# Kernel tuning notes

Measured on AMD Instinct MI355X. Metric: run time of the kernel, lower is better.

## Reference

```python
import jax, jax.numpy as jnp
import numpy as np
from jax import lax

B, C_IN, IMG, P, HID = 128, 3, 224, 16, 768
HW = (IMG // P) ** 2  # 196 patches


def setup_inputs() -> dict:
    key = jax.random.key(0)
    k1, k2, k3, k4 = jax.random.split(key, 4)
    x = jax.random.normal(k1, (B, C_IN, IMG, IMG), dtype=jnp.float32)
    # conv weight init scale ~ kaiming-ish, value irrelevant for correctness
    W = jax.random.normal(k2, (HID, C_IN, P, P), dtype=jnp.float32) * 0.02
    b = jax.random.normal(k3, (HID,), dtype=jnp.float32) * 0.02
    # per-sample random permutation of patch positions (the pixel shuffle)
    perm = jax.vmap(lambda k: jax.random.permutation(k, HW))(jax.random.split(k4, B)).astype(jnp.int32)
    return {"x": x, "W": W, "b": b, "perm": perm}


def reference(x, W, b, perm):
    # patchify conv: kernel_size == stride == P, no padding
    enc = lax.conv_general_dilated(
        x, W, window_strides=(P, P), padding="VALID",
        dimension_numbers=("NCHW", "OIHW", "NCHW"),
    ) + b[None, :, None, None]                      # [B, HID, H', W']
    Bc, Cc, Hc, Wc = enc.shape
    enc = enc.reshape(Bc, Cc, Hc * Wc).transpose(0, 2, 1)   # [B, HW, HID]
    # per-sample patch shuffle: shuffled[i, j] = enc[i, perm[i, j]]
    shuffled = jnp.take_along_axis(enc, perm[:, :, None], axis=1)
    return shuffled
```

## Files before the change

### kernel.cpp

```cpp
#include <hip/hip_runtime.h>
#include <hip/hip_bf16.h>

#define BATCH  128
#define HWN    196
#define HIDN   768
#define KN     768
#define IMGSZ  224
#define IMG2   (224*224)
#define MTOT   (BATCH*HWN)

#define BM 128
#define BN 128
#define BK 32

typedef __attribute__((ext_vector_type(8))) short bf16x8;
typedef __attribute__((ext_vector_type(4))) float floatx4;

#define GP(p) ((const __attribute__((address_space(1))) void*)(p))
#define SP(p) ((__attribute__((address_space(3))) void*)(p))

static __device__ __forceinline__ short f2bf(float f) {
    __hip_bfloat16 h = __float2bfloat16(f);
    return __builtin_bit_cast(short, h);
}

static __device__ __forceinline__ bf16x8 cvt8(const float* __restrict__ src) {
    float4 f0 = *(const float4*)(src);
    float4 f1 = *(const float4*)(src + 4);
    bf16x8 v;
    v[0]=f2bf(f0.x); v[1]=f2bf(f0.y); v[2]=f2bf(f0.z); v[3]=f2bf(f0.w);
    v[4]=f2bf(f1.x); v[5]=f2bf(f1.y); v[6]=f2bf(f1.z); v[7]=f2bf(f1.w);
    return v;
}

__global__ __launch_bounds__(256)
void prep_A(const float* __restrict__ x, const int* __restrict__ perm,
            unsigned short* __restrict__ A)
{
    const int idx = blockIdx.x * 256 + threadIdx.x;
    const int gr  = idx / 48;
    const int seg = idx - gr * 48;
    const int b   = gr / HWN;
    const int p   = perm[gr];
    const int py  = p / 14, px = p - py * 14;
    const int c   = seg >> 4;
    const int iy  = seg & 15;

    const float* src = x + (size_t)b * 3 * IMG2 + (size_t)c * IMG2
                         + (size_t)(py * 16 + iy) * IMGSZ + px * 16;
    bf16x8 v0 = cvt8(src);
    bf16x8 v1 = cvt8(src + 8);
    unsigned short* dst = A + (size_t)gr * KN + seg * 16;
    *(bf16x8*)(dst)     = v0;
    *(bf16x8*)(dst + 8) = v1;
}

__global__ __launch_bounds__(256)
void prep_W(const float* __restrict__ W, unsigned short* __restrict__ Wb)
{
    const int idx = blockIdx.x * 256 + threadIdx.x;
    const float* src = W + (size_t)idx * 8;
    *(bf16x8*)(Wb + (size_t)idx * 8) = cvt8(src);
}

__global__ __launch_bounds__(256, 5)
void gemm(const unsigned short* __restrict__ A, const unsigned short* __restrict__ Wb,
          const float* __restrict__ bias, float* __restrict__ out)
{
    __shared__ __align__(16) unsigned short As[2][BM * BK];
    __shared__ __align__(16) unsigned short Bs[2][BN * BK];

    const int tid = threadIdx.x;

    const int L   = blockIdx.x;
    const int xcd = L & 7;
    const int s   = L >> 3;
    int grp, t;
    if (xcd < 4)        { grp = xcd;     t = s; }
    else if (s < 144)   { grp = xcd;     t = s; }
    else                { grp = xcd - 4; t = 147 + (s - 144); }
    const int bm0 = (grp < 4) ? grp * 25 : 100 + (grp - 4) * 24;
    const int bm  = bm0 + t / 6;
    const int bn  = t % 6;

    const int srow = tid >> 2;
    const int sseg = tid & 3;
    const unsigned short* ga = A  + (size_t)(bm * BM + srow) * KN + sseg * 8;
    const unsigned short* gb = Wb + (size_t)(bn * BN + srow) * KN + sseg * 8;

    const int lane = tid & 63;
    const int wave = tid >> 6;
    const int wm = (wave >> 1) * 64;
    const int wn = (wave & 1) * 64;
    const int lr = lane & 15;
    const int lq = lane >> 4;

    floatx4 acc[4][4] = {};

    auto issue = [&](int k0, int b) {
        __builtin_amdgcn_global_load_lds(GP(ga + k0),           SP(&As[b][tid * 8]),        16, 0, 0);
        __builtin_amdgcn_global_load_lds(GP(ga + 64 * KN + k0), SP(&As[b][2048 + tid * 8]), 16, 0, 0);
        __builtin_amdgcn_global_load_lds(GP(gb + k0),           SP(&Bs[b][tid * 8]),        16, 0, 0);
        __builtin_amdgcn_global_load_lds(GP(gb + 64 * KN + k0), SP(&Bs[b][2048 + tid * 8]), 16, 0, 0);
    };
    auto compute = [&](int b) {
        bf16x8 bfrag[4];
        #pragma unroll
        for (int j = 0; j < 4; ++j)
            bfrag[j] = *(const bf16x8*)&Bs[b][(wn + j * 16 + lr) * BK + lq * 8];
        #pragma unroll
        for (int i = 0; i < 4; ++i) {
            bf16x8 afrag = *(const bf16x8*)&As[b][(wm + i * 16 + lr) * BK + lq * 8];
            #pragma unroll
            for (int j = 0; j < 4; ++j)
                acc[i][j] = __builtin_amdgcn_mfma_f32_16x16x32_bf16(
                                bfrag[j], afrag, acc[i][j], 0, 0, 0);
        }
    };

    issue(0, 0);
    for (int k0 = 0; k0 < KN; k0 += 2 * BK) {
        __syncthreads();
        if (k0 + BK < KN) issue(k0 + BK, 1);
        compute(0);
        __syncthreads();
        if (k0 + 2 * BK < KN) issue(k0 + 2 * BK, 0);
        compute(1);
    }

    #pragma unroll
    for (int j = 0; j < 4; ++j) {
        const int gc0 = bn * BN + wn + j * 16 + lq * 4;
        const float4 bv = *(const float4*)&bias[gc0];
        #pragma unroll
        for (int i = 0; i < 4; ++i) {
            const int grow = bm * BM + wm + i * 16 + lr;
            float4 v;
            v.x = acc[i][j][0] + bv.x;
            v.y = acc[i][j][1] + bv.y;
            v.z = acc[i][j][2] + bv.z;
            v.w = acc[i][j][3] + bv.w;
            *(float4*)(out + (size_t)grow * HIDN + gc0) = v;
        }
    }
}

extern "C" void kernel_launch(void* const* d_in, const int* in_sizes, int n_in,
                              void* d_out, int out_size, void* d_ws, size_t ws_size,
                              hipStream_t stream) {
    const float* x    = (const float*)d_in[0];
    const float* W    = (const float*)d_in[1];
    const float* bias = (const float*)d_in[2];
    const int*   perm = (const int*)d_in[3];
    float* out = (float*)d_out;

    unsigned short* A  = (unsigned short*)d_ws;
    unsigned short* Wb = A + (size_t)MTOT * KN;

    prep_A<<<dim3(MTOT * 48 / 256), dim3(256), 0, stream>>>(x, perm, A);
    prep_W<<<dim3(KN * HIDN / 8 / 256), dim3(256), 0, stream>>>(W, Wb);
    gemm<<<dim3(1176), dim3(256), 0, stream>>>(A, Wb, bias, out);
}
```

Measured before the change: 192.3 us.

## Fuse patch gather and bf16 conversion into GEMM A-tile loading

Drops the separate prep_A kernel. The GEMM now reads fp32 image pixels directly through the permuted patch addresses, converts them to bf16 in registers and writes them into LDS, using a register-prefetch pipeline two k-steps ahead. This removes writing and re-reading a bf16 A matrix of about 38 MB plus one kernel launch. In exchange each A tile is re-read as fp32 by all six N-tile blocks instead of once, more registers are used, and occupancy is lowered to 4 waves per SIMD.

```diff
diff --git a/kernel.cpp b/kernel.cpp
--- a/kernel.cpp
+++ b/kernel.cpp
@@ -12,6 +12,7 @@
 #define BM 128
 #define BN 128
 #define BK 32
+#define NITER (KN / BK)
 
 typedef __attribute__((ext_vector_type(8))) short bf16x8;
 typedef __attribute__((ext_vector_type(4))) float floatx4;
@@ -24,9 +25,7 @@
     return __builtin_bit_cast(short, h);
 }
 
-static __device__ __forceinline__ bf16x8 cvt8(const float* __restrict__ src) {
-    float4 f0 = *(const float4*)(src);
-    float4 f1 = *(const float4*)(src + 4);
+static __device__ __forceinline__ bf16x8 cvt2x4(float4 f0, float4 f1) {
     bf16x8 v;
     v[0]=f2bf(f0.x); v[1]=f2bf(f0.y); v[2]=f2bf(f0.z); v[3]=f2bf(f0.w);
     v[4]=f2bf(f1.x); v[5]=f2bf(f1.y); v[6]=f2bf(f1.z); v[7]=f2bf(f1.w);
@@ -34,38 +33,19 @@
 }
 
 __global__ __launch_bounds__(256)
-void prep_A(const float* __restrict__ x, const int* __restrict__ perm,
-            unsigned short* __restrict__ A)
-{
-    const int idx = blockIdx.x * 256 + threadIdx.x;
-    const int gr  = idx / 48;
-    const int seg = idx - gr * 48;
-    const int b   = gr / HWN;
-    const int p   = perm[gr];
-    const int py  = p / 14, px = p - py * 14;
-    const int c   = seg >> 4;
-    const int iy  = seg & 15;
-
-    const float* src = x + (size_t)b * 3 * IMG2 + (size_t)c * IMG2
-                         + (size_t)(py * 16 + iy) * IMGSZ + px * 16;
-    bf16x8 v0 = cvt8(src);
-    bf16x8 v1 = cvt8(src + 8);
-    unsigned short* dst = A + (size_t)gr * KN + seg * 16;
-    *(bf16x8*)(dst)     = v0;
-    *(bf16x8*)(dst + 8) = v1;
-}
-
-__global__ __launch_bounds__(256)
 void prep_W(const float* __restrict__ W, unsigned short* __restrict__ Wb)
 {
     const int idx = blockIdx.x * 256 + threadIdx.x;
     const float* src = W + (size_t)idx * 8;
-    *(bf16x8*)(Wb + (size_t)idx * 8) = cvt8(src);
+    float4 f0 = *(const float4*)(src);
+    float4 f1 = *(const float4*)(src + 4);
+    *(bf16x8*)(Wb + (size_t)idx * 8) = cvt2x4(f0, f1);
 }
 
-__global__ __launch_bounds__(256, 5)
-void gemm(const unsigned short* __restrict__ A, const unsigned short* __restrict__ Wb,
-          const float* __restrict__ bias, float* __restrict__ out)
+__global__ __launch_bounds__(256, 4)
+void gemm(const float* __restrict__ x, const unsigned short* __restrict__ Wb,
+          const float* __restrict__ bias, const int* __restrict__ perm,
+          float* __restrict__ out)
 {
     __shared__ __align__(16) unsigned short As[2][BM * BK];
     __shared__ __align__(16) unsigned short Bs[2][BN * BK];
@@ -83,10 +63,17 @@
     const int bm  = bm0 + t / 6;
     const int bn  = t % 6;
 
-    const int srow = tid >> 2;
-    const int sseg = tid & 3;
-    const unsigned short* ga = A  + (size_t)(bm * BM + srow) * KN + sseg * 8;
-    const unsigned short* gb = Wb + (size_t)(bn * BN + srow) * KN + sseg * 8;
+    const int arow_i = tid >> 2;
+    const int kseg   = tid & 3;
+    const int gr0 = bm * BM + arow_i;
+    const int gr1 = gr0 + 64;
+    const int p0 = perm[gr0], p1 = perm[gr1];
+    const float* arow0 = x + (size_t)(gr0 / HWN) * 3 * IMG2
+                           + (size_t)((p0 / 14) * 16) * IMGSZ + (p0 % 14) * 16;
+    const float* arow1 = x + (size_t)(gr1 / HWN) * 3 * IMG2
+                           + (size_t)((p1 / 14) * 16) * IMGSZ + (p1 % 14) * 16;
+
+    const unsigned short* gb = Wb + (size_t)(bn * BN + (tid >> 2)) * KN + kseg * 8;
 
     const int lane = tid & 63;
     const int wave = tid >> 6;
@@ -97,11 +84,26 @@
 
     floatx4 acc[4][4] = {};
 
-    auto issue = [&](int k0, int b) {
-        __builtin_amdgcn_global_load_lds(GP(ga + k0),           SP(&As[b][tid * 8]),        16, 0, 0);
-        __builtin_amdgcn_global_load_lds(GP(ga + 64 * KN + k0), SP(&As[b][2048 + tid * 8]), 16, 0, 0);
-        __builtin_amdgcn_global_load_lds(GP(gb + k0),           SP(&Bs[b][tid * 8]),        16, 0, 0);
-        __builtin_amdgcn_global_load_lds(GP(gb + 64 * KN + k0), SP(&Bs[b][2048 + tid * 8]), 16, 0, 0);
+    auto xoff = [&](int k0) {
+        const int kk = k0 + kseg * 8;
+        return (kk >> 8) * IMG2 + (((kk >> 4) & 15) * IMGSZ) + (kk & 15);
+    };
+    auto issueB = [&](int i, int b) {
+        __builtin_amdgcn_global_load_lds(GP(gb + i * BK),           SP(&Bs[b][tid * 8]),        16, 0, 0);
+        __builtin_amdgcn_global_load_lds(GP(gb + 64 * KN + i * BK), SP(&Bs[b][2048 + tid * 8]), 16, 0, 0);
+    };
+
+    float4 f0, f1, f2, f3;
+    auto loadA = [&](int i) {
+        const int off = xoff(i * BK);
+        f0 = *(const float4*)(arow0 + off);
+        f1 = *(const float4*)(arow0 + off + 4);
+        f2 = *(const float4*)(arow1 + off);
+        f3 = *(const float4*)(arow1 + off + 4);
+    };
+    auto writeA = [&](int b) {
+        *(bf16x8*)&As[b][tid * 8]        = cvt2x4(f0, f1);
+        *(bf16x8*)&As[b][2048 + tid * 8] = cvt2x4(f2, f3);
     };
     auto compute = [&](int b) {
         bf16x8 bfrag[4];
@@ -118,14 +120,19 @@
         }
     };
 
-    issue(0, 0);
-    for (int k0 = 0; k0 < KN; k0 += 2 * BK) {
+    loadA(0);
+    issueB(0, 0);
+    writeA(0);
+    loadA(1);
+
+    for (int i = 0; i < NITER; ++i) {
         __syncthreads();
-        if (k0 + BK < KN) issue(k0 + BK, 1);
-        compute(0);
-        __syncthreads();
-        if (k0 + 2 * BK < KN) issue(k0 + 2 * BK, 0);
-        compute(1);
+        if (i + 1 < NITER) {
+            issueB(i + 1, (i + 1) & 1);
+            writeA((i + 1) & 1);
+        }
+        if (i + 2 < NITER) loadA(i + 2);
+        compute(i & 1);
     }
 
     #pragma unroll
@@ -154,10 +161,8 @@
     const int*   perm = (const int*)d_in[3];
     float* out = (float*)d_out;
 
-    unsigned short* A  = (unsigned short*)d_ws;
-    unsigned short* Wb = A + (size_t)MTOT * KN;
+    unsigned short* Wb = (unsigned short*)d_ws;
 
-    prep_A<<<dim3(MTOT * 48 / 256), dim3(256), 0, stream>>>(x, perm, A);
     prep_W<<<dim3(KN * HIDN / 8 / 256), dim3(256), 0, stream>>>(W, Wb);
-    gemm<<<dim3(1176), dim3(256), 0, stream>>>(A, Wb, bias, out);
+    gemm<<<dim3(1176), dim3(256), 0, stream>>>(x, Wb, bias, perm, out);
 }
```

New measurement: 200.5 us. +4.2%, slower.
